# Kernel optimization log

Measured on AMD Instinct MI355X. Metric: run time of the kernel, lower is better.

## Reference

```python
import jax, jax.numpy as jnp
import numpy as np

B = 32768
NMU = 3
K = 8
TMAX = 31.41592653589793
DE = 128
NC = 64
ZC = 1
IN_DIM = K + K * NMU  # 32

FREQS = jnp.asarray(1.0 / (np.float32(TMAX) ** np.arange(K // 2, dtype=np.float32)))


def _sinenc(x):
    # x: (B,) or (B,d) -> (B, K) or (B, d*K); per-feature [sin|cos] blocks concatenated
    if x.ndim == 1:
        xw = x[:, None] * FREQS[None, :]
        return jnp.concatenate([jnp.sin(xw), jnp.cos(xw)], axis=1)
    xw = x[:, :, None] * FREQS[None, None, :]  # (B, d, K/2)
    return jnp.concatenate([jnp.sin(xw), jnp.cos(xw)], axis=2).reshape(x.shape[0], -1)


def _conv3(x, w, b):
    y = jax.lax.conv_general_dilated(x, w, window_strides=(1, 1), padding=((1, 1), (1, 1)),
                                     dimension_numbers=("NCHW", "OIHW", "NCHW"))
    return y + b[None, :, None, None]


def setup_inputs() -> dict:
    key = jax.random.key(0)
    ks = jax.random.split(key, 20)
    s = 0.05
    return {
        "t": jax.random.uniform(ks[0], (B,), jnp.float32) * TMAX,
        "z": jax.random.normal(ks[1], (B, ZC, 4, 4), jnp.float32),
        "mu": jax.random.normal(ks[2], (B, NMU), jnp.float32),
        "W1": jax.random.normal(ks[3], (IN_DIM, DE), jnp.float32) * s,
        "b1": jnp.zeros((DE,), jnp.float32),
        "W2": jax.random.normal(ks[4], (DE, DE), jnp.float32) * s,
        "b2": jnp.zeros((DE,), jnp.float32),
        "Wg": jax.random.normal(ks[5], (DE, 4 * NC), jnp.float32) * s,
        "bg": jnp.zeros((4 * NC,), jnp.float32),
        "cin_w": jax.random.normal(ks[6], (NC, ZC, 3, 3), jnp.float32) * s,
        "cin_b": jnp.zeros((NC,), jnp.float32),
        "c1_w": jax.random.normal(ks[7], (NC, NC, 3, 3), jnp.float32) * s,
        "c1_b": jnp.zeros((NC,), jnp.float32),
        "c2_w": jax.random.normal(ks[8], (NC, NC, 3, 3), jnp.float32) * s,
        "c2_b": jnp.zeros((NC,), jnp.float32),
        "cout_w": jax.random.normal(ks[9], (ZC, NC, 3, 3), jnp.float32) * s,
        "cout_b": jnp.zeros((ZC,), jnp.float32),
    }


def reference(t, z, mu, W1, b1, W2, b2, Wg, bg,
              cin_w, cin_b, c1_w, c1_b, c2_w, c2_b, cout_w, cout_b):
    t_emb = _sinenc(t)            # (B, K)
    mu_emb = _sinenc(mu)          # (B, K*nmu)
    x = jnp.concatenate([t_emb, mu_emb], axis=1)  # (B, in_dim)
    h = jax.nn.elu(x @ W1 + b1)
    xi = jax.nn.elu(h @ W2 + b2)
    gb = (xi @ Wg + bg).reshape(-1, 4, NC)
    g1 = gb[:, 0][:, :, None, None]
    g2 = gb[:, 1][:, :, None, None]
    bb1 = gb[:, 2][:, :, None, None]
    bb2 = gb[:, 3][:, :, None, None]
    hh = jnp.tanh(_conv3(z, cin_w, cin_b))
    hh = jnp.tanh(g1 * _conv3(hh, c1_w, c1_b) + bb1)
    hh = jnp.tanh(g2 * _conv3(hh, c2_w, c2_b) + bb2)
    return _conv3(hh, cout_w, cout_b)
```

## Files before the change

### kernel.cpp

```cpp
#include <hip/hip_runtime.h>
#include <cstdint>
#include <cstddef>


#define NB 32768

typedef _Float16 half8   __attribute__((ext_vector_type(8)));
typedef _Float16 half4_t __attribute__((ext_vector_type(4)));
typedef _Float16 half2_t __attribute__((ext_vector_type(2)));
typedef float    f32x4   __attribute__((ext_vector_type(4)));
typedef float    f32x16  __attribute__((ext_vector_type(16)));

__device__ __forceinline__ float fast_tanh(float x) {
  float e = __expf(2.0f * x);
  return 1.0f - __fdividef(2.0f, e + 1.0f);
}

__device__ __forceinline__ float elu_f(float v) {
  return v > 0.0f ? v : (__expf(v) - 1.0f);
}

__device__ __forceinline__ void conv_acc(float acc[16], const float r[16], const float w[9]) {
#pragma unroll
  for (int y = 0; y < 4; ++y)
#pragma unroll
    for (int x = 0; x < 4; ++x)
#pragma unroll
      for (int ky = 0; ky < 3; ++ky) {
        int iy = y + ky - 1;
        if (iy < 0 || iy >= 4) continue;
#pragma unroll
        for (int kx = 0; kx < 3; ++kx) {
          int ix = x + kx - 1;
          if (ix < 0 || ix >= 4) continue;
          acc[y * 4 + x] += w[ky * 3 + kx] * r[iy * 4 + ix];
        }
      }
}

__global__ __launch_bounds__(256) void prep_kernel(
    const float* __restrict__ W1, const float* __restrict__ W2,
    const float* __restrict__ Wg, const float* __restrict__ c1w,
    const float* __restrict__ c2w, _Float16* __restrict__ wt) {
  int idx = blockIdx.x * 256 + threadIdx.x;
  _Float16* W1f = wt;
  _Float16* W2f = W1f + 4096;
  _Float16* Wgf = W2f + 16384;
  _Float16* c1t = Wgf + 32768;
  _Float16* c2t = c1t + 36864;
  if (idx < 4096) {
    int i = idx, j = i & 7, lane = (i >> 3) & 63, nt = i >> 9;
    int n = nt * 16 + (lane & 15), k = (lane >> 4) * 8 + j;
    W1f[i] = (_Float16)W1[k * 128 + n];
  } else if (idx < 20480) {
    int i = idx - 4096, j = i & 7, lane = (i >> 3) & 63, r = i >> 9;
    int kb = r & 3, nt = r >> 2;
    int n = nt * 16 + (lane & 15), k = kb * 32 + (lane >> 4) * 8 + j;
    W2f[i] = (_Float16)W2[k * 128 + n];
  } else if (idx < 53248) {
    int i = idx - 20480, j = i & 7, lane = (i >> 3) & 63, r = i >> 9;
    int kb = r & 3, ut = r >> 2;
    int n = ut * 16 + (lane & 15), k = kb * 32 + (lane >> 4) * 8 + j;
    Wgf[i] = (_Float16)Wg[k * 256 + n];
  } else if (idx < 90112) {
    int i = idx - 53248;
    int j = i & 7, lane = (i >> 3) & 63, ts = i >> 9;
    int wtile = ts & 1, f = ts >> 1, kb = f & 3, tap = f >> 2;
    int oc = wtile * 32 + (lane & 31);
    int ic = kb * 16 + (lane >> 5) * 8 + j;
    c1t[i] = (_Float16)c1w[(oc * 64 + ic) * 9 + tap];
  } else if (idx < 126976) {
    int i = idx - 90112;
    int j = i & 7, lane = (i >> 3) & 63, ts = i >> 9;
    int wtile = ts & 1, f = ts >> 1, kb = f & 3, tap = f >> 2;
    int oc = wtile * 32 + (lane & 31);
    int ic = kb * 16 + (lane >> 5) * 8 + j;
    c2t[i] = (_Float16)c2w[(oc * 64 + ic) * 9 + tap];
  }
}

#define ROWE 72
#define SAMP 2592
#define SLOT (4 * SAMP)
#define GRPS 16
#define GBROW 264

__device__ __forceinline__ void mid32(
    const _Float16* __restrict__ src, _Float16* __restrict__ dst,
    const half8 af[36], const f32x4 cb[4],
    const _Float16* __restrict__ grow, int goff,
    int wtile, int sp, int lane) {
  const int col = lane & 31, hi = lane >> 5;
  const int px = col & 15, sw = col >> 4;
  const int py = px >> 2, pxx = px & 3;
  const int samp = sp * 2 + sw;
  const _Float16* sbase = src + samp * SAMP;

  f32x16 acc = (f32x16)(0.0f);
#pragma unroll
  for (int tap = 0; tap < 9; ++tap) {
    const int ky = tap / 3, kx = tap % 3;
    const int row = py + ky;
    const int pos = row * 6 + pxx + kx;
    const int e = (row ^ (pos >> 2)) & 1;
#pragma unroll
    for (int kb = 0; kb < 4; ++kb) {
      const int ic0 = kb * 16 + hi * 8;
      const int off = pos * ROWE + ((((ic0 >> 5) ^ e) << 5)) + (ic0 & 31);
      half8 b = *(const half8*)(sbase + off);
      acc = __builtin_amdgcn_mfma_f32_32x32x16_f16(af[tap * 4 + kb], b, acc, 0, 0, 0);
    }
  }

  const int row_i = 1 + py;
  const int pos_i = row_i * 6 + 1 + pxx;
  const int e_i = (row_i ^ (pos_i >> 2)) & 1;
  _Float16* dbase = dst + samp * SAMP + pos_i * ROWE + ((wtile ^ e_i) << 5);
  const _Float16* gp = grow + samp * GBROW + goff;
#pragma unroll
  for (int g4 = 0; g4 < 4; ++g4) {
    const int ocb = 8 * g4 + 4 * hi;
    const int oc = wtile * 32 + ocb;
    half4_t gv = *(const half4_t*)(gp + oc);
    half4_t bv = *(const half4_t*)(gp + 128 + oc);
    half4_t o;
#pragma unroll
    for (int r = 0; r < 4; ++r)
      o[r] = (_Float16)fast_tanh((float)gv[r] * (acc[4 * g4 + r] + cb[g4][r]) + (float)bv[r]);
    *(half4_t*)(dbase + ocb) = o;
  }
}

__global__ __launch_bounds__(512, 1) void fused_kernel(
    const float* __restrict__ tt, const float* __restrict__ mu,
    const float* __restrict__ z, const _Float16* __restrict__ wt,
    const float* __restrict__ b1, const float* __restrict__ b2,
    const float* __restrict__ bg,
    const float* __restrict__ cin_w, const float* __restrict__ cin_b,
    const float* __restrict__ c1_b, const float* __restrict__ c2_b,
    const float* __restrict__ cout_w, const float* __restrict__ cout_b,
    float* __restrict__ out) {
  const int tid = threadIdx.x;
  const int lane = tid & 63;
  const int wid = tid >> 6;
  const bool isC2 = (wid >= 4);
  const int w4 = wid & 3;
  const int wtile = w4 & 1;
  const int sp = w4 >> 1;
  const int s0 = blockIdx.x * (GRPS * 4);

  const _Float16* W1f = wt;
  const _Float16* W2f = W1f + 4096;
  const _Float16* Wgf = W2f + 16384;
  const _Float16* c1t = Wgf + 32768;
  const _Float16* c2t = c1t + 36864;

  __shared__ __align__(16) _Float16 hp[4 * SLOT];
  __shared__ __align__(16) _Float16 gb_lds[64 * GBROW];
  __shared__ __align__(16) _Float16 cwl[9 * 64];

  const int m = lane & 15, q = lane >> 4, q8 = q * 8, q4 = q * 4;
  const int py16 = m >> 2, px16 = m & 3;

  const _Float16* at = isC2 ? c2t : c1t;
  half8 af[36];
#pragma unroll
  for (int f = 0; f < 36; ++f)
    af[f] = *(const half8*)(at + ((f * 2 + wtile) << 9) + lane * 8);

  const float* cbsrc = isC2 ? c2_b : c1_b;
  f32x4 cbv[4];
#pragma unroll
  for (int g4 = 0; g4 < 4; ++g4)
    cbv[g4] = *(const f32x4*)(cbsrc + wtile * 32 + 8 * g4 + 4 * (lane >> 5));

  float cw9[9];
  float cinb = 0.0f;
  if (!isC2) {
#pragma unroll
    for (int t = 0; t < 9; ++t) cw9[t] = cin_w[lane * 9 + t];
    cinb = cin_b[lane];
  } else {
    for (int i = tid - 256; i < 576; i += 256) {
      if (i >= 0) {
        int ic = i / 9, tap = i % 9;
        cwl[tap * 64 + ic] = (_Float16)cout_w[i];
      }
    }
  }
  const float cob = cout_b[0];

  if (!isC2) {
    const int sl = wid * 16 + m;
    const int s = s0 + sl;
    _Float16* xw = hp + wid * SAMP;

    const float TM = 31.41592653589793f;
    float base = (q == 0) ? tt[s] : mu[(size_t)s * 3 + (q - 1)];
    half8 xb;
    float fr = 1.0f;
#pragma unroll
    for (int j = 0; j < 4; ++j) {
      float sn, cs;
      __sincosf(base * fr, &sn, &cs);
      xb[j] = (_Float16)sn;
      xb[4 + j] = (_Float16)cs;
      fr *= (1.0f / TM);
    }

#pragma unroll
    for (int nt = 0; nt < 8; ++nt) {
      half8 a = *(const half8*)(W1f + (nt * 64 + lane) * 8);
      f32x4 c = __builtin_amdgcn_mfma_f32_16x16x32_f16(a, xb, (f32x4)(0.0f), 0, 0, 0);
      f32x4 bv = *(const f32x4*)(b1 + nt * 16 + q4);
      half4_t o;
#pragma unroll
      for (int r = 0; r < 4; ++r) o[r] = (_Float16)elu_f(c[r] + bv[r]);
      *(half4_t*)(xw + m * 136 + nt * 16 + q4) = o;
    }
    half8 xf0 = *(const half8*)(xw + m * 136 + 0 + q8);
    half8 xf1 = *(const half8*)(xw + m * 136 + 32 + q8);
    half8 xf2 = *(const half8*)(xw + m * 136 + 64 + q8);
    half8 xf3 = *(const half8*)(xw + m * 136 + 96 + q8);

#pragma unroll
    for (int nt = 0; nt < 8; ++nt) {
      const _Float16* wp = W2f + (nt * 4) * 512 + lane * 8;
      f32x4 c = (f32x4)(0.0f);
      c = __builtin_amdgcn_mfma_f32_16x16x32_f16(*(const half8*)(wp), xf0, c, 0, 0, 0);
      c = __builtin_amdgcn_mfma_f32_16x16x32_f16(*(const half8*)(wp + 512), xf1, c, 0, 0, 0);
      c = __builtin_amdgcn_mfma_f32_16x16x32_f16(*(const half8*)(wp + 1024), xf2, c, 0, 0, 0);
      c = __builtin_amdgcn_mfma_f32_16x16x32_f16(*(const half8*)(wp + 1536), xf3, c, 0, 0, 0);
      f32x4 bv = *(const f32x4*)(b2 + nt * 16 + q4);
      half4_t o;
#pragma unroll
      for (int r = 0; r < 4; ++r) o[r] = (_Float16)elu_f(c[r] + bv[r]);
      *(half4_t*)(xw + m * 136 + nt * 16 + q4) = o;
    }
    half8 yf0 = *(const half8*)(xw + m * 136 + 0 + q8);
    half8 yf1 = *(const half8*)(xw + m * 136 + 32 + q8);
    half8 yf2 = *(const half8*)(xw + m * 136 + 64 + q8);
    half8 yf3 = *(const half8*)(xw + m * 136 + 96 + q8);

#pragma unroll
    for (int ut = 0; ut < 16; ++ut) {
      const _Float16* wp = Wgf + (ut * 4) * 512 + lane * 8;
      f32x4 c = (f32x4)(0.0f);
      c = __builtin_amdgcn_mfma_f32_16x16x32_f16(*(const half8*)(wp), yf0, c, 0, 0, 0);
      c = __builtin_amdgcn_mfma_f32_16x16x32_f16(*(const half8*)(wp + 512), yf1, c, 0, 0, 0);
      c = __builtin_amdgcn_mfma_f32_16x16x32_f16(*(const half8*)(wp + 1024), yf2, c, 0, 0, 0);
      c = __builtin_amdgcn_mfma_f32_16x16x32_f16(*(const half8*)(wp + 1536), yf3, c, 0, 0, 0);
      f32x4 bv = *(const f32x4*)(bg + ut * 16 + q4);
      half4_t o;
#pragma unroll
      for (int r = 0; r < 4; ++r) o[r] = (_Float16)(c[r] + bv[r]);
      *(half4_t*)(gb_lds + sl * GBROW + ut * 16 + q4) = o;
    }
  }
  __syncthreads();

  {
    uint32_t* hp32 = (uint32_t*)hp;
    for (int i = tid; i < (4 * SLOT) / 2; i += 512) hp32[i] = 0u;
  }
  __syncthreads();

  for (int it = 0; it <= GRPS; ++it) {
    if (!isC2) {
      if (it < GRPS) {
        const float* zp = z + (size_t)(s0 + it * 4 + w4) * 16;
        float r[16], acc[16];
#pragma unroll
        for (int p = 0; p < 16; ++p) { r[p] = zp[p]; acc[p] = 0.0f; }
        conv_acc(acc, r, cw9);
        _Float16* dst = hp + (it & 1) * SLOT + w4 * SAMP;
        const int ics = lane & 31, ich = lane >> 5;
#pragma unroll
        for (int p = 0; p < 16; ++p) {
          int row = 1 + (p >> 2);
          int pos = row * 6 + 1 + (p & 3);
          int e = (row ^ (pos >> 2)) & 1;
          dst[pos * ROWE + ((ich ^ e) << 5) + ics] = (_Float16)fast_tanh(acc[p] + cinb);
        }
      }
    } else {
      if (it >= 1) {
        const int j = (it - 1) & 1;
        mid32(hp + (2 + j) * SLOT, hp + j * SLOT, af, cbv,
              gb_lds + (size_t)((it - 1) * 4) * GBROW, 64, wtile, sp, lane);
      }
    }
    __syncthreads();

    if (!isC2) {
      if (it < GRPS) {
        const int j = it & 1;
        mid32(hp + j * SLOT, hp + (2 + j) * SLOT, af, cbv,
              gb_lds + (size_t)(it * 4) * GBROW, 0, wtile, sp, lane);
      }
    } else {
      if (it >= 1) {
        const _Float16* src = hp + ((it - 1) & 1) * SLOT + w4 * SAMP;
        const int c32 = q >> 1;
        const int coff = (q * 16) & 31;
        float acc = 0.0f;
#pragma unroll
        for (int tap = 0; tap < 9; ++tap) {
          const int ky = tap / 3, kx = tap % 3;
          const int row = py16 + ky;
          const int pos = row * 6 + px16 + kx;
          const int e = (row ^ (pos >> 2)) & 1;
          const _Float16* spp = src + pos * ROWE + ((c32 ^ e) << 5) + coff;
          half8 hv0 = *(const half8*)(spp);
          half8 hv1 = *(const half8*)(spp + 8);
          half8 wv0 = *(const half8*)(cwl + tap * 64 + q * 16);
          half8 wv1 = *(const half8*)(cwl + tap * 64 + q * 16 + 8);
#pragma unroll
          for (int jj = 0; jj < 4; ++jj) {
            half2_t h2a = {hv0[2 * jj], hv0[2 * jj + 1]};
            half2_t w2a = {wv0[2 * jj], wv0[2 * jj + 1]};
            half2_t h2b = {hv1[2 * jj], hv1[2 * jj + 1]};
            half2_t w2b = {wv1[2 * jj], wv1[2 * jj + 1]};
#if __has_builtin(__builtin_amdgcn_fdot2)
            acc = __builtin_amdgcn_fdot2(h2a, w2a, acc, false);
            acc = __builtin_amdgcn_fdot2(h2b, w2b, acc, false);
#else
            acc += (float)h2a[0] * (float)w2a[0] + (float)h2a[1] * (float)w2a[1];
            acc += (float)h2b[0] * (float)w2b[0] + (float)h2b[1] * (float)w2b[1];
#endif
          }
        }
        acc += __shfl_xor(acc, 16);
        acc += __shfl_xor(acc, 32);
        if (q == 0) out[(size_t)(s0 + (it - 1) * 4 + w4) * 16 + m] = acc + cob;
      }
    }
    __syncthreads();
  }
}

extern "C" void kernel_launch(void* const* d_in, const int* in_sizes, int n_in,
                              void* d_out, int out_size, void* d_ws, size_t ws_size,
                              hipStream_t stream) {
  const float* tt     = (const float*)d_in[0];
  const float* z      = (const float*)d_in[1];
  const float* mu     = (const float*)d_in[2];
  const float* W1     = (const float*)d_in[3];
  const float* b1     = (const float*)d_in[4];
  const float* W2     = (const float*)d_in[5];
  const float* b2     = (const float*)d_in[6];
  const float* Wg     = (const float*)d_in[7];
  const float* bg     = (const float*)d_in[8];
  const float* cin_w  = (const float*)d_in[9];
  const float* cin_b  = (const float*)d_in[10];
  const float* c1_w   = (const float*)d_in[11];
  const float* c1_b   = (const float*)d_in[12];
  const float* c2_w   = (const float*)d_in[13];
  const float* c2_b   = (const float*)d_in[14];
  const float* cout_w = (const float*)d_in[15];
  const float* cout_b = (const float*)d_in[16];

  float* out = (float*)d_out;
  _Float16* wt = (_Float16*)d_ws;

  prep_kernel<<<496, 256, 0, stream>>>(W1, W2, Wg, c1_w, c2_w, wt);
  fused_kernel<<<NB / 64, 512, 0, stream>>>(
      tt, mu, z, wt, b1, b2, bg, cin_w, cin_b, c1_b, c2_b, cout_w, cout_b, out);
}
```

Baseline: 269.9 us.

## Halve block to four waves, each processing two samples per stage

The fused kernel now launches 256 threads instead of 512. Each wave handles two samples or spatial halves of the conv stages instead of one. All four waves now run the MLP/gating prologue, and the cout weight staging moves into the zero-fill pass. The aim is smaller blocks so more of them can be co-resident per CU, letting one block's barriers overlap another's work. The cost is twice the serial work per wave within each pipeline step and possible register pressure from the doubled loops.

```diff
diff --git a/kernel.cpp b/kernel.cpp
--- a/kernel.cpp
+++ b/kernel.cpp
@@ -131,7 +131,7 @@
   }
 }
 
-__global__ __launch_bounds__(512, 1) void fused_kernel(
+__global__ __launch_bounds__(256, 1) void fused_kernel(
     const float* __restrict__ tt, const float* __restrict__ mu,
     const float* __restrict__ z, const _Float16* __restrict__ wt,
     const float* __restrict__ b1, const float* __restrict__ b2,
@@ -143,10 +143,9 @@
   const int tid = threadIdx.x;
   const int lane = tid & 63;
   const int wid = tid >> 6;
-  const bool isC2 = (wid >= 4);
-  const int w4 = wid & 3;
-  const int wtile = w4 & 1;
-  const int sp = w4 >> 1;
+  const bool isC2 = (wid >= 2);
+  const int wtile = wid & 1;
+  const int wpair = isC2 ? (wid - 2) : wid;
   const int s0 = blockIdx.x * (GRPS * 4);
 
   const _Float16* W1f = wt;
@@ -162,35 +161,7 @@
   const int m = lane & 15, q = lane >> 4, q8 = q * 8, q4 = q * 4;
   const int py16 = m >> 2, px16 = m & 3;
 
-  const _Float16* at = isC2 ? c2t : c1t;
-  half8 af[36];
-#pragma unroll
-  for (int f = 0; f < 36; ++f)
-    af[f] = *(const half8*)(at + ((f * 2 + wtile) << 9) + lane * 8);
-
-  const float* cbsrc = isC2 ? c2_b : c1_b;
-  f32x4 cbv[4];
-#pragma unroll
-  for (int g4 = 0; g4 < 4; ++g4)
-    cbv[g4] = *(const f32x4*)(cbsrc + wtile * 32 + 8 * g4 + 4 * (lane >> 5));
-
-  float cw9[9];
-  float cinb = 0.0f;
-  if (!isC2) {
-#pragma unroll
-    for (int t = 0; t < 9; ++t) cw9[t] = cin_w[lane * 9 + t];
-    cinb = cin_b[lane];
-  } else {
-    for (int i = tid - 256; i < 576; i += 256) {
-      if (i >= 0) {
-        int ic = i / 9, tap = i % 9;
-        cwl[tap * 64 + ic] = (_Float16)cout_w[i];
-      }
-    }
-  }
-  const float cob = cout_b[0];
-
-  if (!isC2) {
+  {
     const int sl = wid * 16 + m;
     const int s = s0 + sl;
     _Float16* xw = hp + wid * SAMP;
@@ -259,35 +230,67 @@
   }
   __syncthreads();
 
+  const _Float16* at = isC2 ? c2t : c1t;
+  half8 af[36];
+#pragma unroll
+  for (int f = 0; f < 36; ++f)
+    af[f] = *(const half8*)(at + ((f * 2 + wtile) << 9) + lane * 8);
+
+  const float* cbsrc = isC2 ? c2_b : c1_b;
+  f32x4 cbv[4];
+#pragma unroll
+  for (int g4 = 0; g4 < 4; ++g4)
+    cbv[g4] = *(const f32x4*)(cbsrc + wtile * 32 + 8 * g4 + 4 * (lane >> 5));
+
+  float cw9[9];
+  float cinb = 0.0f;
+  if (!isC2) {
+#pragma unroll
+    for (int t = 0; t < 9; ++t) cw9[t] = cin_w[lane * 9 + t];
+    cinb = cin_b[lane];
+  }
+  const float cob = cout_b[0];
+
   {
     uint32_t* hp32 = (uint32_t*)hp;
-    for (int i = tid; i < (4 * SLOT) / 2; i += 512) hp32[i] = 0u;
+    for (int i = tid; i < (4 * SLOT) / 2; i += 256) hp32[i] = 0u;
+    for (int i = tid; i < 576; i += 256) {
+      int ic = i / 9, tap = i % 9;
+      cwl[tap * 64 + ic] = (_Float16)cout_w[i];
+    }
   }
   __syncthreads();
 
   for (int it = 0; it <= GRPS; ++it) {
     if (!isC2) {
       if (it < GRPS) {
-        const float* zp = z + (size_t)(s0 + it * 4 + w4) * 16;
-        float r[16], acc[16];
-#pragma unroll
-        for (int p = 0; p < 16; ++p) { r[p] = zp[p]; acc[p] = 0.0f; }
-        conv_acc(acc, r, cw9);
-        _Float16* dst = hp + (it & 1) * SLOT + w4 * SAMP;
+        _Float16* dstbase = hp + (it & 1) * SLOT;
         const int ics = lane & 31, ich = lane >> 5;
 #pragma unroll
-        for (int p = 0; p < 16; ++p) {
-          int row = 1 + (p >> 2);
-          int pos = row * 6 + 1 + (p & 3);
-          int e = (row ^ (pos >> 2)) & 1;
-          dst[pos * ROWE + ((ich ^ e) << 5) + ics] = (_Float16)fast_tanh(acc[p] + cinb);
+        for (int s2 = 0; s2 < 2; ++s2) {
+          const int samp = wpair * 2 + s2;
+          const float* zp = z + (size_t)(s0 + it * 4 + samp) * 16;
+          float r[16], acc[16];
+#pragma unroll
+          for (int p = 0; p < 16; ++p) { r[p] = zp[p]; acc[p] = 0.0f; }
+          conv_acc(acc, r, cw9);
+          _Float16* dst = dstbase + samp * SAMP;
+#pragma unroll
+          for (int p = 0; p < 16; ++p) {
+            int row = 1 + (p >> 2);
+            int pos = row * 6 + 1 + (p & 3);
+            int e = (row ^ (pos >> 2)) & 1;
+            dst[pos * ROWE + ((ich ^ e) << 5) + ics] = (_Float16)fast_tanh(acc[p] + cinb);
+          }
         }
       }
     } else {
       if (it >= 1) {
         const int j = (it - 1) & 1;
         mid32(hp + (2 + j) * SLOT, hp + j * SLOT, af, cbv,
-              gb_lds + (size_t)((it - 1) * 4) * GBROW, 64, wtile, sp, lane);
+              gb_lds + (size_t)((it - 1) * 4) * GBROW, 64, wtile, 0, lane);
+        mid32(hp + (2 + j) * SLOT, hp + j * SLOT, af, cbv,
+              gb_lds + (size_t)((it - 1) * 4) * GBROW, 64, wtile, 1, lane);
       }
     }
     __syncthreads();
@@ -296,43 +299,50 @@
       if (it < GRPS) {
         const int j = it & 1;
         mid32(hp + j * SLOT, hp + (2 + j) * SLOT, af, cbv,
-              gb_lds + (size_t)(it * 4) * GBROW, 0, wtile, sp, lane);
+              gb_lds + (size_t)(it * 4) * GBROW, 0, wtile, 0, lane);
+        mid32(hp + j * SLOT, hp + (2 + j) * SLOT, af, cbv,
+              gb_lds + (size_t)(it * 4) * GBROW, 0, wtile, 1, lane);
       }
     } else {
       if (it >= 1) {
-        const _Float16* src = hp + ((it - 1) & 1) * SLOT + w4 * SAMP;
+        const _Float16* srcbase = hp + ((it - 1) & 1) * SLOT;
         const int c32 = q >> 1;
         const int coff = (q * 16) & 31;
-        float acc = 0.0f;
-#pragma unroll
-        for (int tap = 0; tap < 9; ++tap) {
-          const int ky = tap / 3, kx = tap % 3;
-          const int row = py16 + ky;
-          const int pos = row * 6 + px16 + kx;
-          const int e = (row ^ (pos >> 2)) & 1;
-          const _Float16* spp = src + pos * ROWE + ((c32 ^ e) << 5) + coff;
-          half8 hv0 = *(const half8*)(spp);
-          half8 hv1 = *(const half8*)(spp + 8);
-          half8 wv0 = *(const half8*)(cwl + tap * 64 + q * 16);
-          half8 wv1 = *(const half8*)(cwl + tap * 64 + q * 16 + 8);
-#pragma unroll
-          for (int jj = 0; jj < 4; ++jj) {
-            half2_t h2a = {hv0[2 * jj], hv0[2 * jj + 1]};
-            half2_t w2a = {wv0[2 * jj], wv0[2 * jj + 1]};
-            half2_t h2b = {hv1[2 * jj], hv1[2 * jj + 1]};
-            half2_t w2b = {wv1[2 * jj], wv1[2 * jj + 1]};
+#pragma unroll
+        for (int s2 = 0; s2 < 2; ++s2) {
+          const int samp = wpair * 2 + s2;
+          const _Float16* src = srcbase + samp * SAMP;
+          float acc = 0.0f;
+#pragma unroll
+          for (int tap = 0; tap < 9; ++tap) {
+            const int ky = tap / 3, kx = tap % 3;
+            const int row = py16 + ky;
+            const int pos = row * 6 + px16 + kx;
+            const int e = (row ^ (pos >> 2)) & 1;
+            const _Float16* spp = src + pos * ROWE + ((c32 ^ e) << 5) + coff;
+            half8 hv0 = *(const half8*)(spp);
+            half8 hv1 = *(const half8*)(spp + 8);
+            half8 wv0 = *(const half8*)(cwl + tap * 64 + q * 16);
+            half8 wv1 = *(const half8*)(cwl + tap * 64 + q * 16 + 8);
+#pragma unroll
+            for (int jj = 0; jj < 4; ++jj) {
+              half2_t h2a = {hv0[2 * jj], hv0[2 * jj + 1]};
+              half2_t w2a = {wv0[2 * jj], wv0[2 * jj + 1]};
+              half2_t h2b = {hv1[2 * jj], hv1[2 * jj + 1]};
+              half2_t w2b = {wv1[2 * jj], wv1[2 * jj + 1]};
 #if __has_builtin(__builtin_amdgcn_fdot2)
-            acc = __builtin_amdgcn_fdot2(h2a, w2a, acc, false);
-            acc = __builtin_amdgcn_fdot2(h2b, w2b, acc, false);
+              acc = __builtin_amdgcn_fdot2(h2a, w2a, acc, false);
+              acc = __builtin_amdgcn_fdot2(h2b, w2b, acc, false);
 #else
-            acc += (float)h2a[0] * (float)w2a[0] + (float)h2a[1] * (float)w2a[1];
-            acc += (float)h2b[0] * (float)w2b[0] + (float)h2b[1] * (float)w2b[1];
+              acc += (float)h2a[0] * (float)w2a[0] + (float)h2a[1] * (float)w2a[1];
+              acc += (float)h2b[0] * (float)w2b[0] + (float)h2b[1] * (float)w2b[1];
 #endif
+            }
           }
+          acc += __shfl_xor(acc, 16);
+          acc += __shfl_xor(acc, 32);
+          if (q == 0) out[(size_t)(s0 + (it - 1) * 4 + samp) * 16 + m] = acc + cob;
         }
-        acc += __shfl_xor(acc, 16);
-        acc += __shfl_xor(acc, 32);
-        if (q == 0) out[(size_t)(s0 + (it - 1) * 4 + w4) * 16 + m] = acc + cob;
       }
     }
     __syncthreads();
@@ -364,6 +374,6 @@
   _Float16* wt = (_Float16*)d_ws;
 
   prep_kernel<<<496, 256, 0, stream>>>(W1, W2, Wg, c1_w, c2_w, wt);
-  fused_kernel<<<NB / 64, 512, 0, stream>>>(
+  fused_kernel<<<NB / 64, 256, 0, stream>>>(
       tt, mu, z, wt, b1, b2, bg, cin_w, cin_b, c1_b, c2_b, cout_w, cout_b, out);
 }
```

Result: slower. 329.9 us (+22.3%).

## Replace warp-specialized c1/c2 pipeline with 256-thread blocks streaming weights from memory

Applied to the files above, without the earlier changes.

Drops the 8-wave design, where half the waves held c1 weights and half held c2 weights in registers and ran as a two-stage pipeline. Each block now has 4 waves that run cin, c1, c2 and cout in sequence per group of 4 samples. MFMA A-fragments are loaded from global/L2 on every tap instead of staying in registers. The aim is to cut register and LDS pressure so two blocks fit per CU, at the cost of extra weight load traffic and losing the overlap between the c1 and c2 stages.

```diff
diff --git a/kernel.cpp b/kernel.cpp
--- a/kernel.cpp
+++ b/kernel.cpp
@@ -81,13 +81,13 @@
 
 #define ROWE 72
 #define SAMP 2592
-#define SLOT (4 * SAMP)
+#define GS 4
 #define GRPS 16
 #define GBROW 264
 
 __device__ __forceinline__ void mid32(
     const _Float16* __restrict__ src, _Float16* __restrict__ dst,
-    const half8 af[36], const f32x4 cb[4],
+    const _Float16* __restrict__ at, const f32x4 cb[4],
     const _Float16* __restrict__ grow, int goff,
     int wtile, int sp, int lane) {
   const int col = lane & 31, hi = lane >> 5;
@@ -95,6 +95,7 @@
   const int py = px >> 2, pxx = px & 3;
   const int samp = sp * 2 + sw;
   const _Float16* sbase = src + samp * SAMP;
+  const _Float16* abase = at + wtile * 512 + lane * 8;
 
   f32x16 acc = (f32x16)(0.0f);
 #pragma unroll
@@ -107,8 +108,9 @@
     for (int kb = 0; kb < 4; ++kb) {
       const int ic0 = kb * 16 + hi * 8;
       const int off = pos * ROWE + ((((ic0 >> 5) ^ e) << 5)) + (ic0 & 31);
+      half8 a = *(const half8*)(abase + ((tap * 4 + kb) << 10));
       half8 b = *(const half8*)(sbase + off);
-      acc = __builtin_amdgcn_mfma_f32_32x32x16_f16(af[tap * 4 + kb], b, acc, 0, 0, 0);
+      acc = __builtin_amdgcn_mfma_f32_32x32x16_f16(a, b, acc, 0, 0, 0);
     }
   }
 
@@ -131,7 +133,7 @@
   }
 }
 
-__global__ __launch_bounds__(512, 1) void fused_kernel(
+__global__ __launch_bounds__(256, 2) void fused_kernel(
     const float* __restrict__ tt, const float* __restrict__ mu,
     const float* __restrict__ z, const _Float16* __restrict__ wt,
     const float* __restrict__ b1, const float* __restrict__ b2,
@@ -143,11 +145,9 @@
   const int tid = threadIdx.x;
   const int lane = tid & 63;
   const int wid = tid >> 6;
-  const bool isC2 = (wid >= 4);
-  const int w4 = wid & 3;
-  const int wtile = w4 & 1;
-  const int sp = w4 >> 1;
-  const int s0 = blockIdx.x * (GRPS * 4);
+  const int wtile = wid & 1;
+  const int sp = wid >> 1;
+  const int s0 = blockIdx.x * (GRPS * GS);
 
   const _Float16* W1f = wt;
   const _Float16* W2f = W1f + 4096;
@@ -155,42 +155,14 @@
   const _Float16* c1t = Wgf + 32768;
   const _Float16* c2t = c1t + 36864;
 
-  __shared__ __align__(16) _Float16 hp[4 * SLOT];
+  __shared__ __align__(16) _Float16 hp[2 * GS * SAMP];
   __shared__ __align__(16) _Float16 gb_lds[64 * GBROW];
   __shared__ __align__(16) _Float16 cwl[9 * 64];
 
   const int m = lane & 15, q = lane >> 4, q8 = q * 8, q4 = q * 4;
   const int py16 = m >> 2, px16 = m & 3;
 
-  const _Float16* at = isC2 ? c2t : c1t;
-  half8 af[36];
-#pragma unroll
-  for (int f = 0; f < 36; ++f)
-    af[f] = *(const half8*)(at + ((f * 2 + wtile) << 9) + lane * 8);
-
-  const float* cbsrc = isC2 ? c2_b : c1_b;
-  f32x4 cbv[4];
-#pragma unroll
-  for (int g4 = 0; g4 < 4; ++g4)
-    cbv[g4] = *(const f32x4*)(cbsrc + wtile * 32 + 8 * g4 + 4 * (lane >> 5));
-
-  float cw9[9];
-  float cinb = 0.0f;
-  if (!isC2) {
-#pragma unroll
-    for (int t = 0; t < 9; ++t) cw9[t] = cin_w[lane * 9 + t];
-    cinb = cin_b[lane];
-  } else {
-    for (int i = tid - 256; i < 576; i += 256) {
-      if (i >= 0) {
-        int ic = i / 9, tap = i % 9;
-        cwl[tap * 64 + ic] = (_Float16)cout_w[i];
-      }
-    }
-  }
-  const float cob = cout_b[0];
-
-  if (!isC2) {
+  {
     const int sl = wid * 16 + m;
     const int s = s0 + sl;
     _Float16* xw = hp + wid * SAMP;
@@ -257,83 +229,94 @@
       *(half4_t*)(gb_lds + sl * GBROW + ut * 16 + q4) = o;
     }
   }
+
+  float cw9[9];
+#pragma unroll
+  for (int t = 0; t < 9; ++t) cw9[t] = cin_w[lane * 9 + t];
+  const float cinb = cin_b[lane];
+  const float cob = cout_b[0];
+
+  f32x4 cb1[4], cb2[4];
+#pragma unroll
+  for (int g4 = 0; g4 < 4; ++g4) {
+    cb1[g4] = *(const f32x4*)(c1_b + wtile * 32 + 8 * g4 + 4 * (lane >> 5));
+    cb2[g4] = *(const f32x4*)(c2_b + wtile * 32 + 8 * g4 + 4 * (lane >> 5));
+  }
+
   __syncthreads();
 
   {
     uint32_t* hp32 = (uint32_t*)hp;
-    for (int i = tid; i < (4 * SLOT) / 2; i += 512) hp32[i] = 0u;
+    for (int i = tid; i < (2 * GS * SAMP) / 2; i += 256) hp32[i] = 0u;
+    for (int i = tid; i < 576; i += 256) {
+      int ic = i / 9, tap = i % 9;
+      cwl[tap * 64 + ic] = (_Float16)cout_w[i];
+    }
   }
   __syncthreads();
 
-  for (int it = 0; it <= GRPS; ++it) {
-    if (!isC2) {
-      if (it < GRPS) {
-        const float* zp = z + (size_t)(s0 + it * 4 + w4) * 16;
-        float r[16], acc[16];
-#pragma unroll
-        for (int p = 0; p < 16; ++p) { r[p] = zp[p]; acc[p] = 0.0f; }
-        conv_acc(acc, r, cw9);
-        _Float16* dst = hp + (it & 1) * SLOT + w4 * SAMP;
-        const int ics = lane & 31, ich = lane >> 5;
-#pragma unroll
-        for (int p = 0; p < 16; ++p) {
-          int row = 1 + (p >> 2);
-          int pos = row * 6 + 1 + (p & 3);
-          int e = (row ^ (pos >> 2)) & 1;
-          dst[pos * ROWE + ((ich ^ e) << 5) + ics] = (_Float16)fast_tanh(acc[p] + cinb);
+  for (int grp = 0; grp < GRPS; ++grp) {
+    const int sg = s0 + grp * GS;
+    const _Float16* gbase = gb_lds + (size_t)(grp * GS) * GBROW;
+
+    {
+      const float* zp = z + (size_t)(sg + wid) * 16;
+      float r[16], acc[16];
+#pragma unroll
+      for (int p = 0; p < 16; ++p) { r[p] = zp[p]; acc[p] = 0.0f; }
+      conv_acc(acc, r, cw9);
+      _Float16* dst = hp + wid * SAMP;
+      const int ics = lane & 31, ich = lane >> 5;
+#pragma unroll
+      for (int p = 0; p < 16; ++p) {
+        int row = 1 + (p >> 2);
+        int pos = row * 6 + 1 + (p & 3);
+        int e = (row ^ (pos >> 2)) & 1;
+        dst[pos * ROWE + ((ich ^ e) << 5) + ics] = (_Float16)fast_tanh(acc[p] + cinb);
+      }
+    }
+    __syncthreads();
+
+    mid32(hp, hp + GS * SAMP, c1t, cb1, gbase, 0, wtile, sp, lane);
+    __syncthreads();
+
+    mid32(hp + GS * SAMP, hp, c2t, cb2, gbase, 64, wtile, sp, lane);
+    __syncthreads();
+
+    {
+      const _Float16* src = hp + wid * SAMP;
+      const int c32 = q >> 1;
+      const int coff = (q * 16) & 31;
+      float acc = 0.0f;
+#pragma unroll
+      for (int tap = 0; tap < 9; ++tap) {
+        const int ky = tap / 3, kx = tap % 3;
+        const int row = py16 + ky;
+        const int pos = row * 6 + px16 + kx;
+        const int e = (row ^ (pos >> 2)) & 1;
+        const _Float16* spp = src + pos * ROWE + ((c32 ^ e) << 5) + coff;
+        half8 hv0 = *(const half8*)(spp);
+        half8 hv1 = *(const half8*)(spp + 8);
+        half8 wv0 = *(const half8*)(cwl + tap * 64 + q * 16);
+        half8 wv1 = *(const half8*)(cwl + tap * 64 + q * 16 + 8);
+#pragma unroll
+        for (int jj = 0; jj < 4; ++jj) {
+          half2_t h2a = {hv0[2 * jj], hv0[2 * jj + 1]};
+          half2_t w2a = {wv0[2 * jj], wv0[2 * jj + 1]};
+          half2_t h2b = {hv1[2 * jj], hv1[2 * jj + 1]};
+          half2_t w2b = {wv1[2 * jj], wv1[2 * jj + 1]};
+#if __has_builtin(__builtin_amdgcn_fdot2)
+          acc = __builtin_amdgcn_fdot2(h2a, w2a, acc, false);
+          acc = __builtin_amdgcn_fdot2(h2b, w2b, acc, false);
+#else
+          acc += (float)h2a[0] * (float)w2a[0] + (float)h2a[1] * (float)w2a[1];
+          acc += (float)h2b[0] * (float)w2b[0] + (float)h2b[1] * (float)w2b[1];
+#endif
         }
       }
-    } else {
-      if (it >= 1) {
-        const int j = (it - 1) & 1;
-        mid32(hp + (2 + j) * SLOT, hp + j * SLOT, af, cbv,
-              gb_lds + (size_t)((it - 1) * 4) * GBROW, 64, wtile, sp, lane);
-      }
-    }
-    __syncthreads();
-
-    if (!isC2) {
-      if (it < GRPS) {
-        const int j = it & 1;
-        mid32(hp + j * SLOT, hp + (2 + j) * SLOT, af, cbv,
-              gb_lds + (size_t)(it * 4) * GBROW, 0, wtile, sp, lane);
-      }
-    } else {
-      if (it >= 1) {
-        const _Float16* src = hp + ((it - 1) & 1) * SLOT + w4 * SAMP;
-        const int c32 = q >> 1;
-        const int coff = (q * 16) & 31;
-        float acc = 0.0f;
-#pragma unroll
-        for (int tap = 0; tap < 9; ++tap) {
-          const int ky = tap / 3, kx = tap % 3;
-          const int row = py16 + ky;
-          const int pos = row * 6 + px16 + kx;
-          const int e = (row ^ (pos >> 2)) & 1;
-          const _Float16* spp = src + pos * ROWE + ((c32 ^ e) << 5) + coff;
-          half8 hv0 = *(const half8*)(spp);
-          half8 hv1 = *(const half8*)(spp + 8);
-          half8 wv0 = *(const half8*)(cwl + tap * 64 + q * 16);
-          half8 wv1 = *(const half8*)(cwl + tap * 64 + q * 16 + 8);
-#pragma unroll
-          for (int jj = 0; jj < 4; ++jj) {
-            half2_t h2a = {hv0[2 * jj], hv0[2 * jj + 1]};
-            half2_t w2a = {wv0[2 * jj], wv0[2 * jj + 1]};
-            half2_t h2b = {hv1[2 * jj], hv1[2 * jj + 1]};
-            half2_t w2b = {wv1[2 * jj], wv1[2 * jj + 1]};
-#if __has_builtin(__builtin_amdgcn_fdot2)
-            acc = __builtin_amdgcn_fdot2(h2a, w2a, acc, false);
-            acc = __builtin_amdgcn_fdot2(h2b, w2b, acc, false);
-#else
-            acc += (float)h2a[0] * (float)w2a[0] + (float)h2a[1] * (float)w2a[1];
-            acc += (float)h2b[0] * (float)w2b[0] + (float)h2b[1] * (float)w2b[1];
-#endif
-          }
-        }
-        acc += __shfl_xor(acc, 16);
-        acc += __shfl_xor(acc, 32);
-        if (q == 0) out[(size_t)(s0 + (it - 1) * 4 + w4) * 16 + m] = acc + cob;
-      }
+      acc += __shfl_xor(acc, 16);
+      acc += __shfl_xor(acc, 32);
+      if (q == 0) out[(size_t)(sg + wid) * 16 + m] = acc + cob;
     }
     __syncthreads();
   }
@@ -364,6 +347,6 @@
   _Float16* wt = (_Float16*)d_ws;
 
   prep_kernel<<<496, 256, 0, stream>>>(W1, W2, Wg, c1_w, c2_w, wt);
-  fused_kernel<<<NB / 64, 512, 0, stream>>>(
+  fused_kernel<<<NB / 64, 256, 0, stream>>>(
       tt, mu, z, wt, b1, b2, bg, cin_w, cin_b, c1_b, c2_b, cout_w, cout_b, out);
 }
```

New measurement: 377.7 us. 1.4x slower.
